# Performance work log

Hardware: AMD Instinct MI355X
Metric: run time of the kernel (lower is better)

The kernel has to match this reference:

```python
import jax, jax.numpy as jnp
import numpy as np

N, E, D, H = 8192, 8, 2048, 2048


def setup_inputs() -> dict:
    key = jax.random.key(0)
    k1, k2, k3, k4 = jax.random.split(key, 4)
    x = jax.random.normal(k1, (N, D), dtype=jnp.float32)
    indices = jax.random.randint(k2, (N, 1), 0, E)  # top_k=1 expert assignment
    W = jax.random.normal(k3, (E, D, H), dtype=jnp.float32) * 0.02
    b = jax.random.normal(k4, (E, H), dtype=jnp.float32) * 0.02
    return {"x": x, "indices": indices, "W": W, "b": b}


def reference(x, indices, W, b):
    # Each token is routed to exactly one expert (top_k=1):
    # expert_id[n] = indices[n, 0]. The torch module loops experts e=0..E-1,
    # gathers tokens with (indices == e).any(-1) (ascending order via nonzero),
    # applies expert e's Linear + ReLU, and concatenates outputs in expert order.
    expert_id = indices[:, 0]                              # [N]
    # Dense dispatch: compute every expert's linear on every token, then pick
    # each token's own expert row (jit-friendly; no data-dependent shapes).
    y_all = jnp.einsum('nd,edh->neh', x, W) + b[None, :, :]  # [N, E, H]
    y = jnp.take_along_axis(y_all, expert_id[:, None, None], axis=1)[:, 1 - 1, :]  # [N, H]
    y = jax.nn.relu(y)
    # Concat in expert order == stable sort of tokens by expert id
    # (nonzero returns ascending indices, so within-expert order is preserved).
    order = jnp.argsort(expert_id)  # stable by default
    return y[order]
```

## Files before the change

kernel.cpp:

```cpp
#include <hip/hip_runtime.h>

#define N_TOK 8192
#define N_EXP 8
#define DIM   2048
#define HID   2048

typedef __attribute__((ext_vector_type(8))) short short8;
typedef __attribute__((ext_vector_type(4))) float f32x4;
typedef __attribute__((ext_vector_type(4))) unsigned short ushort4v;

__device__ inline unsigned short f2bf(float f) {
  unsigned int u = __builtin_bit_cast(unsigned int, f);
  unsigned int r = u + 0x7FFFu + ((u >> 16) & 1u);
  return (unsigned short)(r >> 16);
}

__global__ __launch_bounds__(256) void sort_experts(const int* __restrict__ idx,
                                                    int* __restrict__ perm,
                                                    int* __restrict__ offs) {
  __shared__ int cnt[256][8];
  __shared__ int base[8];
  const int t = threadIdx.x;
  int local[8] = {0,0,0,0,0,0,0,0};
  const int r0 = t * 32;
  for (int i = 0; i < 32; ++i) {
    int e = idx[r0 + i] & 7;
    ++local[e];
  }
#pragma unroll
  for (int e = 0; e < 8; ++e) cnt[t][e] = local[e];
  __syncthreads();
  if (t < 8) {
    int s = 0;
    for (int i = 0; i < 256; ++i) { int v = cnt[i][t]; cnt[i][t] = s; s += v; }
    base[t] = s;
  }
  __syncthreads();
  if (t == 0) {
    int s = 0;
    for (int e = 0; e < 8; ++e) { int v = base[e]; offs[e] = s; base[e] = s; s += v; }
    offs[8] = s;
  }
  __syncthreads();
  int pos[8];
#pragma unroll
  for (int e = 0; e < 8; ++e) pos[e] = base[e] + cnt[t][e];
  for (int i = 0; i < 32; ++i) {
    int r = r0 + i;
    int e = idx[r] & 7;
    perm[pos[e]++] = r;
  }
}

__global__ __launch_bounds__(256) void gather_convert_x(const float* __restrict__ x,
                                                        const int* __restrict__ perm,
                                                        unsigned short* __restrict__ xs) {
  int gid = blockIdx.x * 256 + threadIdx.x;
  int p = gid >> 8;
  int c = gid & 255;
  int src = perm[p];
  const float* sp = x + (size_t)src * DIM + c * 8;
  float4 a = *(const float4*)sp;
  float4 b = *(const float4*)(sp + 4);
  short8 o;
  o[0] = (short)f2bf(a.x); o[1] = (short)f2bf(a.y);
  o[2] = (short)f2bf(a.z); o[3] = (short)f2bf(a.w);
  o[4] = (short)f2bf(b.x); o[5] = (short)f2bf(b.y);
  o[6] = (short)f2bf(b.z); o[7] = (short)f2bf(b.w);
  *(short8*)(xs + (size_t)p * DIM + c * 8) = o;
}

__global__ __launch_bounds__(256) void transpose_convert_w(const float* __restrict__ W,
                                                           unsigned short* __restrict__ Wt) {
  __shared__ unsigned short tile[64][68];
  const int e = blockIdx.z;
  const int d0 = blockIdx.y * 64;
  const int h0 = blockIdx.x * 64;
  const int t = threadIdx.x;
  const int cr = t & 15;
  const int rr = t >> 4;
  const float* Wp = W + ((size_t)e * DIM + d0) * HID + h0;
#pragma unroll
  for (int i = 0; i < 4; ++i) {
    int d = rr + i * 16;
    float4 v = *(const float4*)(Wp + (size_t)d * HID + cr * 4);
    ushort4v o;
    o[0] = f2bf(v.x); o[1] = f2bf(v.y); o[2] = f2bf(v.z); o[3] = f2bf(v.w);
    *(ushort4v*)&tile[d][cr * 4] = o;
  }
  __syncthreads();
  unsigned short* op = Wt + ((size_t)e * HID + h0) * DIM + d0;
#pragma unroll
  for (int i = 0; i < 4; ++i) {
    int h = rr + i * 16;
    ushort4v o;
    o[0] = tile[cr * 4 + 0][h];
    o[1] = tile[cr * 4 + 1][h];
    o[2] = tile[cr * 4 + 2][h];
    o[3] = tile[cr * 4 + 3][h];
    *(ushort4v*)(op + (size_t)h * DIM + cr * 4) = o;
  }
}

#define BM 128
#define BN 128
#define BK 32

__global__ __launch_bounds__(256) void grouped_gemm(const unsigned short* __restrict__ xs,
                                                    const unsigned short* __restrict__ Wt,
                                                    const float* __restrict__ bias,
                                                    const int* __restrict__ offs,
                                                    float* __restrict__ out) {
  const int e   = blockIdx.z;
  const int off = offs[e];
  const int cnt = offs[e + 1] - off;
  const int mt  = blockIdx.y;
  if (mt * BM >= cnt) return;
  const int n0 = blockIdx.x * BN;

  __shared__ __align__(16) unsigned short As[BM * BK];
  __shared__ __align__(16) unsigned short Bs[BN * BK];

  const int t    = threadIdx.x;
  const int wid  = t >> 6;
  const int lane = t & 63;
  const int wr   = wid >> 1, wc = wid & 1;
  const int l15  = lane & 15;
  const int l4   = lane >> 4;

  f32x4 acc[4][4] = {};

  size_t srcA[2], srcB[2];
  const size_t WtE = (size_t)e * DIM * HID;
#pragma unroll
  for (int c = 0; c < 2; ++c) {
    int lin = c * 256 + t;
    int r = lin >> 2, kq = lin & 3;
    int p = off + mt * BM + r;
    if (p > N_TOK - 1) p = N_TOK - 1;
    srcA[c] = (size_t)p * DIM + kq * 8;
    srcB[c] = WtE + (size_t)(n0 + r) * DIM + kq * 8;
  }

  for (int k0 = 0; k0 < DIM; k0 += BK) {
#pragma unroll
    for (int c = 0; c < 2; ++c) {
      __builtin_amdgcn_global_load_lds(
          (const __attribute__((address_space(1))) void*)(xs + srcA[c] + k0),
          (__attribute__((address_space(3))) void*)(As + c * 2048 + t * 8), 16, 0, 0);
      __builtin_amdgcn_global_load_lds(
          (const __attribute__((address_space(1))) void*)(Wt + srcB[c] + k0),
          (__attribute__((address_space(3))) void*)(Bs + c * 2048 + t * 8), 16, 0, 0);
    }
    __syncthreads();

    short8 af[4], bf[4];
#pragma unroll
    for (int m = 0; m < 4; ++m) {
      int row = wr * 64 + m * 16 + l15;
      af[m] = *(const short8*)(As + row * BK + l4 * 8);
    }
#pragma unroll
    for (int n = 0; n < 4; ++n) {
      int row = wc * 64 + n * 16 + l15;
      bf[n] = *(const short8*)(Bs + row * BK + l4 * 8);
    }
#pragma unroll
    for (int m = 0; m < 4; ++m)
#pragma unroll
      for (int n = 0; n < 4; ++n)
        acc[m][n] = __builtin_amdgcn_mfma_f32_16x16x32_bf16(af[m], bf[n], acc[m][n], 0, 0, 0);
    __syncthreads();
  }

#pragma unroll
  for (int n = 0; n < 4; ++n) {
    int col = n0 + wc * 64 + n * 16 + l15;
    float bv = bias[e * HID + col];
#pragma unroll
    for (int m = 0; m < 4; ++m) {
#pragma unroll
      for (int q = 0; q < 4; ++q) {
        int rl = wr * 64 + m * 16 + l4 * 4 + q;
        if (mt * BM + rl < cnt) {
          float v = acc[m][n][q] + bv;
          out[(size_t)(off + mt * BM + rl) * HID + col] = v > 0.f ? v : 0.f;
        }
      }
    }
  }
}

extern "C" void kernel_launch(void* const* d_in, const int* in_sizes, int n_in,
                              void* d_out, int out_size, void* d_ws, size_t ws_size,
                              hipStream_t stream) {
  const float* x   = (const float*)d_in[0];
  const int*   idx = (const int*)d_in[1];
  const float* W   = (const float*)d_in[2];
  const float* b   = (const float*)d_in[3];
  float* out = (float*)d_out;

  char* ws = (char*)d_ws;
  unsigned short* xs = (unsigned short*)ws;
  unsigned short* Wt = (unsigned short*)(ws + (size_t)N_TOK * DIM * 2);
  int* perm = (int*)(ws + (size_t)N_TOK * DIM * 2 + (size_t)N_EXP * DIM * HID * 2);
  int* offs = perm + N_TOK;

  sort_experts<<<1, 256, 0, stream>>>(idx, perm, offs);
  gather_convert_x<<<N_TOK * (DIM / 8) / 256, 256, 0, stream>>>(x, perm, xs);
  transpose_convert_w<<<dim3(HID / 64, DIM / 64, N_EXP), 256, 0, stream>>>(W, Wt);
  grouped_gemm<<<dim3(HID / BN, N_TOK / BM, N_EXP), 256, 0, stream>>>(xs, Wt, b, offs, out);
}
```

Baseline: 188.6 us.

## Persistent per-wave grouped GEMM with XCD-aware atomic queue and fused prep

Replaces the 3D-grid grouped GEMM with a persistent kernel. Each wave computes a 64x128 output tile, loading operands straight from global memory into registers with no LDS staging or barriers, and takes its next job from a per-XCD atomic counter. The sort kernel now emits a list of 64-row bands per expert, and column tiles are tied to the XCD so weight slices stay in that XCD's cache. The x gather/convert and W transpose/convert kernels are merged into one launch. The risk is that without LDS staging, memory latency and repeated global reads may be exposed behind an unroll-1 k-loop.

```diff
diff --git a/kernel.cpp b/kernel.cpp
--- a/kernel.cpp
+++ b/kernel.cpp
@@ -17,7 +17,9 @@
 
 __global__ __launch_bounds__(256) void sort_experts(const int* __restrict__ idx,
                                                     int* __restrict__ perm,
-                                                    int* __restrict__ offs) {
+                                                    int* __restrict__ offs,
+                                                    int* __restrict__ bands,
+                                                    int* __restrict__ qcnt) {
   __shared__ int cnt[256][8];
   __shared__ int base[8];
   const int t = threadIdx.x;
@@ -34,12 +36,20 @@
     int s = 0;
     for (int i = 0; i < 256; ++i) { int v = cnt[i][t]; cnt[i][t] = s; s += v; }
     base[t] = s;
+    qcnt[t] = 256;
   }
   __syncthreads();
   if (t == 0) {
-    int s = 0;
-    for (int e = 0; e < 8; ++e) { int v = base[e]; offs[e] = s; base[e] = s; s += v; }
+    int s = 0, nb = 0;
+    for (int e = 0; e < 8; ++e) {
+      int v = base[e];
+      offs[e] = s; base[e] = s;
+      int nm = (v + 63) >> 6;
+      for (int mt = 0; mt < nm; ++mt) bands[1 + nb++] = e | ((s + mt * 64) << 8);
+      s += v;
+    }
     offs[8] = s;
+    bands[0] = nb;
   }
   __syncthreads();
   int pos[8];
@@ -52,142 +62,140 @@
   }
 }
 
-__global__ __launch_bounds__(256) void gather_convert_x(const float* __restrict__ x,
-                                                        const int* __restrict__ perm,
-                                                        unsigned short* __restrict__ xs) {
-  int gid = blockIdx.x * 256 + threadIdx.x;
-  int p = gid >> 8;
-  int c = gid & 255;
-  int src = perm[p];
-  const float* sp = x + (size_t)src * DIM + c * 8;
-  float4 a = *(const float4*)sp;
-  float4 b = *(const float4*)(sp + 4);
-  short8 o;
-  o[0] = (short)f2bf(a.x); o[1] = (short)f2bf(a.y);
-  o[2] = (short)f2bf(a.z); o[3] = (short)f2bf(a.w);
-  o[4] = (short)f2bf(b.x); o[5] = (short)f2bf(b.y);
-  o[6] = (short)f2bf(b.z); o[7] = (short)f2bf(b.w);
-  *(short8*)(xs + (size_t)p * DIM + c * 8) = o;
-}
-
-__global__ __launch_bounds__(256) void transpose_convert_w(const float* __restrict__ W,
-                                                           unsigned short* __restrict__ Wt) {
+__global__ __launch_bounds__(256) void prep(const float* __restrict__ x,
+                                            const int* __restrict__ perm,
+                                            unsigned short* __restrict__ xs,
+                                            const float* __restrict__ W,
+                                            unsigned short* __restrict__ Wt) {
   __shared__ unsigned short tile[64][68];
-  const int e = blockIdx.z;
-  const int d0 = blockIdx.y * 64;
-  const int h0 = blockIdx.x * 64;
   const int t = threadIdx.x;
-  const int cr = t & 15;
-  const int rr = t >> 4;
-  const float* Wp = W + ((size_t)e * DIM + d0) * HID + h0;
-#pragma unroll
-  for (int i = 0; i < 4; ++i) {
-    int d = rr + i * 16;
-    float4 v = *(const float4*)(Wp + (size_t)d * HID + cr * 4);
-    ushort4v o;
-    o[0] = f2bf(v.x); o[1] = f2bf(v.y); o[2] = f2bf(v.z); o[3] = f2bf(v.w);
-    *(ushort4v*)&tile[d][cr * 4] = o;
-  }
-  __syncthreads();
-  unsigned short* op = Wt + ((size_t)e * HID + h0) * DIM + d0;
-#pragma unroll
-  for (int i = 0; i < 4; ++i) {
-    int h = rr + i * 16;
-    ushort4v o;
-    o[0] = tile[cr * 4 + 0][h];
-    o[1] = tile[cr * 4 + 1][h];
-    o[2] = tile[cr * 4 + 2][h];
-    o[3] = tile[cr * 4 + 3][h];
-    *(ushort4v*)(op + (size_t)h * DIM + cr * 4) = o;
-  }
-}
-
-#define BM 128
-#define BN 128
-#define BK 32
-
-__global__ __launch_bounds__(256) void grouped_gemm(const unsigned short* __restrict__ xs,
-                                                    const unsigned short* __restrict__ Wt,
-                                                    const float* __restrict__ bias,
-                                                    const int* __restrict__ offs,
-                                                    float* __restrict__ out) {
-  const int e   = blockIdx.z;
-  const int off = offs[e];
-  const int cnt = offs[e + 1] - off;
-  const int mt  = blockIdx.y;
-  if (mt * BM >= cnt) return;
-  const int n0 = blockIdx.x * BN;
-
-  __shared__ __align__(16) unsigned short As[BM * BK];
-  __shared__ __align__(16) unsigned short Bs[BN * BK];
-
+  if (blockIdx.x < 8192) {
+    int gid = blockIdx.x * 256 + t;
+    int p = gid >> 8;
+    int c = gid & 255;
+    int src = perm[p];
+    const float* sp = x + (size_t)src * DIM + c * 8;
+    float4 a = *(const float4*)sp;
+    float4 b = *(const float4*)(sp + 4);
+    short8 o;
+    o[0] = (short)f2bf(a.x); o[1] = (short)f2bf(a.y);
+    o[2] = (short)f2bf(a.z); o[3] = (short)f2bf(a.w);
+    o[4] = (short)f2bf(b.x); o[5] = (short)f2bf(b.y);
+    o[6] = (short)f2bf(b.z); o[7] = (short)f2bf(b.w);
+    *(short8*)(xs + (size_t)p * DIM + c * 8) = o;
+  } else {
+    const int b = blockIdx.x - 8192;
+    const int e  = b >> 10;
+    const int d0 = ((b >> 5) & 31) * 64;
+    const int h0 = (b & 31) * 64;
+    const int cr = t & 15;
+    const int rr = t >> 4;
+    const float* Wp = W + ((size_t)e * DIM + d0) * HID + h0;
+#pragma unroll
+    for (int i = 0; i < 4; ++i) {
+      int d = rr + i * 16;
+      float4 v = *(const float4*)(Wp + (size_t)d * HID + cr * 4);
+      ushort4v o;
+      o[0] = f2bf(v.x); o[1] = f2bf(v.y); o[2] = f2bf(v.z); o[3] = f2bf(v.w);
+      *(ushort4v*)&tile[d][cr * 4] = o;
+    }
+    __syncthreads();
+    unsigned short* op = Wt + ((size_t)e * HID + h0) * DIM + d0;
+#pragma unroll
+    for (int i = 0; i < 4; ++i) {
+      int h = rr + i * 16;
+      ushort4v o;
+      o[0] = tile[cr * 4 + 0][h];
+      o[1] = tile[cr * 4 + 1][h];
+      o[2] = tile[cr * 4 + 2][h];
+      o[3] = tile[cr * 4 + 3][h];
+      *(ushort4v*)(op + (size_t)h * DIM + cr * 4) = o;
+    }
+  }
+}
+
+#define MM(D,A,B) D = __builtin_amdgcn_mfma_f32_16x16x32_bf16(A, B, D, 0, 0, 0)
+
+__global__ __launch_bounds__(256, 2) void grouped_gemm(
+    const unsigned short* __restrict__ xs,
+    const unsigned short* __restrict__ Wt,
+    const float* __restrict__ bias,
+    const int* __restrict__ offs,
+    const int* __restrict__ bands,
+    int* __restrict__ qcnt,
+    float* __restrict__ out) {
   const int t    = threadIdx.x;
-  const int wid  = t >> 6;
   const int lane = t & 63;
-  const int wr   = wid >> 1, wc = wid & 1;
+  const int w    = t >> 6;
   const int l15  = lane & 15;
   const int l4   = lane >> 4;
-
-  f32x4 acc[4][4] = {};
-
-  size_t srcA[2], srcB[2];
-  const size_t WtE = (size_t)e * DIM * HID;
-#pragma unroll
-  for (int c = 0; c < 2; ++c) {
-    int lin = c * 256 + t;
-    int r = lin >> 2, kq = lin & 3;
-    int p = off + mt * BM + r;
-    if (p > N_TOK - 1) p = N_TOK - 1;
-    srcA[c] = (size_t)p * DIM + kq * 8;
-    srcB[c] = WtE + (size_t)(n0 + r) * DIM + kq * 8;
-  }
-
-  for (int k0 = 0; k0 < DIM; k0 += BK) {
-#pragma unroll
-    for (int c = 0; c < 2; ++c) {
-      __builtin_amdgcn_global_load_lds(
-          (const __attribute__((address_space(1))) void*)(xs + srcA[c] + k0),
-          (__attribute__((address_space(3))) void*)(As + c * 2048 + t * 8), 16, 0, 0);
-      __builtin_amdgcn_global_load_lds(
-          (const __attribute__((address_space(1))) void*)(Wt + srcB[c] + k0),
-          (__attribute__((address_space(3))) void*)(Bs + c * 2048 + t * 8), 16, 0, 0);
-    }
-    __syncthreads();
-
-    short8 af[4], bf[4];
-#pragma unroll
-    for (int m = 0; m < 4; ++m) {
-      int row = wr * 64 + m * 16 + l15;
-      af[m] = *(const short8*)(As + row * BK + l4 * 8);
-    }
-#pragma unroll
-    for (int n = 0; n < 4; ++n) {
-      int row = wc * 64 + n * 16 + l15;
-      bf[n] = *(const short8*)(Bs + row * BK + l4 * 8);
-    }
+  const int xcd  = blockIdx.x & 7;
+
+  const int nj = bands[0] * 2;
+  int i = (blockIdx.x >> 3) * 4 + w;
+
+  while (i < nj) {
+    const int bd   = bands[1 + (i >> 1)];
+    const int e    = bd & 255;
+    const int aRow = bd >> 8;
+    const int hi   = offs[e + 1];
+    const int nx   = (xcd << 1) | (i & 1);
+    const int n0   = nx * 128;
+
+    const unsigned short* pA = xs + (unsigned)(aRow + l15) * 2048u + l4 * 8;
+    const unsigned short* pB = Wt + (size_t)e * ((size_t)DIM * HID)
+                                  + (unsigned)(n0 + l15) * 2048u + l4 * 8;
+
+    f32x4 acc[4][8];
 #pragma unroll
     for (int m = 0; m < 4; ++m)
 #pragma unroll
-      for (int n = 0; n < 4; ++n)
-        acc[m][n] = __builtin_amdgcn_mfma_f32_16x16x32_bf16(af[m], bf[n], acc[m][n], 0, 0, 0);
-    __syncthreads();
-  }
-
-#pragma unroll
-  for (int n = 0; n < 4; ++n) {
-    int col = n0 + wc * 64 + n * 16 + l15;
-    float bv = bias[e * HID + col];
-#pragma unroll
-    for (int m = 0; m < 4; ++m) {
-#pragma unroll
-      for (int q = 0; q < 4; ++q) {
-        int rl = wr * 64 + m * 16 + l4 * 4 + q;
-        if (mt * BM + rl < cnt) {
-          float v = acc[m][n][q] + bv;
-          out[(size_t)(off + mt * BM + rl) * HID + col] = v > 0.f ? v : 0.f;
+      for (int n = 0; n < 8; ++n) acc[m][n] = (f32x4){0.f, 0.f, 0.f, 0.f};
+
+#pragma unroll 1
+    for (int k = 0; k < 2048; k += 32) {
+      short8 fa0 = *(const short8*)(pA + 0 * 32768 + k);
+      short8 fa1 = *(const short8*)(pA + 1 * 32768 + k);
+      short8 fa2 = *(const short8*)(pA + 2 * 32768 + k);
+      short8 fa3 = *(const short8*)(pA + 3 * 32768 + k);
+      short8 fb0 = *(const short8*)(pB + 0 * 32768 + k);
+      short8 fb1 = *(const short8*)(pB + 1 * 32768 + k);
+      short8 fb2 = *(const short8*)(pB + 2 * 32768 + k);
+      short8 fb3 = *(const short8*)(pB + 3 * 32768 + k);
+      short8 fb4 = *(const short8*)(pB + 4 * 32768 + k);
+      short8 fb5 = *(const short8*)(pB + 5 * 32768 + k);
+      short8 fb6 = *(const short8*)(pB + 6 * 32768 + k);
+      short8 fb7 = *(const short8*)(pB + 7 * 32768 + k);
+#pragma unroll
+      for (int m = 0; m < 4; ++m) {
+        const short8 fa = (m == 0) ? fa0 : (m == 1) ? fa1 : (m == 2) ? fa2 : fa3;
+        MM(acc[m][0], fa, fb0); MM(acc[m][1], fa, fb1);
+        MM(acc[m][2], fa, fb2); MM(acc[m][3], fa, fb3);
+        MM(acc[m][4], fa, fb4); MM(acc[m][5], fa, fb5);
+        MM(acc[m][6], fa, fb6); MM(acc[m][7], fa, fb7);
+      }
+    }
+
+#pragma unroll
+    for (int n = 0; n < 8; ++n) {
+      int col = n0 + n * 16 + l15;
+      float bv = bias[e * HID + col];
+#pragma unroll
+      for (int m = 0; m < 4; ++m) {
+#pragma unroll
+        for (int q = 0; q < 4; ++q) {
+          int r = aRow + m * 16 + l4 * 4 + q;
+          if (r < hi) {
+            float v = acc[m][n][q] + bv;
+            out[(size_t)r * HID + col] = v > 0.f ? v : 0.f;
+          }
         }
       }
     }
+
+    int nx_i = 0;
+    if (lane == 0) nx_i = atomicAdd(&qcnt[xcd], 1);
+    i = __shfl(nx_i, 0);
   }
 }
 
@@ -203,11 +211,12 @@
   char* ws = (char*)d_ws;
   unsigned short* xs = (unsigned short*)ws;
   unsigned short* Wt = (unsigned short*)(ws + (size_t)N_TOK * DIM * 2);
-  int* perm = (int*)(ws + (size_t)N_TOK * DIM * 2 + (size_t)N_EXP * DIM * HID * 2);
-  int* offs = perm + N_TOK;
-
-  sort_experts<<<1, 256, 0, stream>>>(idx, perm, offs);
-  gather_convert_x<<<N_TOK * (DIM / 8) / 256, 256, 0, stream>>>(x, perm, xs);
-  transpose_convert_w<<<dim3(HID / 64, DIM / 64, N_EXP), 256, 0, stream>>>(W, Wt);
-  grouped_gemm<<<dim3(HID / BN, N_TOK / BM, N_EXP), 256, 0, stream>>>(xs, Wt, b, offs, out);
-}
+  int* perm  = (int*)(ws + (size_t)N_TOK * DIM * 2 + (size_t)N_EXP * DIM * HID * 2);
+  int* offs  = perm + N_TOK;
+  int* bands = offs + 16;
+  int* qcnt  = bands + 4096;
+
+  sort_experts<<<1, 256, 0, stream>>>(idx, perm, offs, bands, qcnt);
+  prep<<<16384, 256, 0, stream>>>(x, perm, xs, W, Wt);
+  grouped_gemm<<<512, 256, 0, stream>>>(xs, Wt, b, offs, bands, qcnt, out);
+}
```

New measurement: 350.8 us. +86.0%, slower.
